# Performance work log

Measured on AMD Instinct MI355X. Metric: run time of the kernel, lower is better.

## Reference

```python
import jax, jax.numpy as jnp
from jax import lax
import numpy as np

B, H, W = 8, 160, 256
C, K = 700, 250
N_BINS = 750
N_HIST, N_JIT = 30, 60
N_FRAMES = N_HIST + N_JIT
MAGIC = 400.0 / (750.0 - 500.0 + 500.0)


def setup_inputs() -> dict:
    key = jax.random.key(0)
    ks = jax.random.split(key, 10)
    n_pix = H * W
    return {
        "batched_image": jax.random.normal(ks[0], (B, H, W), jnp.float32),
        "batched_spikes": jax.random.uniform(ks[1], (B, C, N_BINS), jnp.float32),
        "eye_movements": jax.random.randint(ks[2], (B, N_JIT, 2), 0, 15),
        "time_mask": jax.random.uniform(ks[3], (B, N_BINS - K), jnp.float32),
        "forward_sel": jax.random.randint(ks[4], (B, N_BINS, 2), 0, N_FRAMES),
        "forward_weights": jax.random.uniform(ks[5], (B, N_BINS, 2), jnp.float32),
        # scale filters so the generator signal stays O(1) under exp() nonlinearity
        "stacked_flat_spat_filters": jax.random.normal(ks[6], (C, n_pix), jnp.float32) / np.sqrt(n_pix).astype(np.float32),
        "stacked_timecourse_filters": jax.random.normal(ks[7], (C, K), jnp.float32) / np.sqrt(K).astype(np.float32),
        "precomputed_feedback_gensig": 0.1 * jax.random.normal(ks[8], (B, C, N_BINS - K + 1), jnp.float32),
        "precomputed_history_frames": jax.random.normal(ks[9], (B, N_HIST, C), jnp.float32),
    }


def _jitter(image, eye_movements):
    # image: (B,H,W); eye_movements: (B,F,2) int shifts. Gather with zero fill.
    dy, dx = eye_movements[..., 0], eye_movements[..., 1]
    rows = jnp.arange(H)[None, None, :] + dy[:, :, None]      # (B,F,H)
    cols = jnp.arange(W)[None, None, :] + dx[:, :, None]      # (B,F,W)
    vr = (rows >= 0) & (rows < H)
    vc = (cols >= 0) & (cols < W)
    rc = jnp.clip(rows, 0, H - 1)
    cc = jnp.clip(cols, 0, W - 1)
    bidx = jnp.arange(image.shape[0])[:, None, None, None]
    jit = image[bidx, rc[:, :, :, None], cc[:, :, None, :]]   # (B,F,H,W)
    mask = (vr[:, :, :, None] & vc[:, :, None, :]).astype(image.dtype)
    return jit * mask


def reference(batched_image, batched_spikes, eye_movements, time_mask,
              forward_sel, forward_weights, stacked_flat_spat_filters,
              stacked_timecourse_filters, precomputed_feedback_gensig,
              precomputed_history_frames):
    b = batched_image.shape[0]
    # eye-movement jitter (gather)
    jit = _jitter(batched_image, eye_movements)                       # (B,Fj,H,W)
    jit_flat = jit.reshape(b, -1, H * W)                              # (B,Fj,P)
    spat_j = jnp.einsum('cp,bfp->bfc', stacked_flat_spat_filters, jit_flat)
    spat = jnp.concatenate([precomputed_history_frames, spat_j], axis=1)  # (B,Ftot,C)
    # interval-overlap time upsample: each bin mixes <=2 frames
    t = forward_sel.shape[1]
    gath = jnp.take_along_axis(spat, forward_sel.reshape(b, t * 2, 1), axis=1)
    gath = gath.reshape(b, t, 2, -1)                                  # (B,T,2,C)
    upsampled = jnp.einsum('btjc,btj->bct', gath, forward_weights)    # (B,C,T)
    # grouped (depthwise) conv1d, valid, no flip (cross-correlation like torch)
    time_filt = lax.conv_general_dilated(
        upsampled, stacked_timecourse_filters[:, None, :],
        window_strides=(1,), padding='VALID',
        dimension_numbers=('NCH', 'OIH', 'NCH'), feature_group_count=C)  # (B,C,T-K+1)
    gen_sig = time_filt + precomputed_feedback_gensig
    g = gen_sig[:, :, :-1]
    s = batched_spikes[:, :, K:]
    loss = jnp.exp(g) - s * g                                          # Poisson NLL (unnormed)
    loss = loss * time_mask[:, None, :] * MAGIC
    return jnp.sum(loss, axis=(1, 2))
```

## Files before the change

kernel.cpp:

```cpp
#include <hip/hip_runtime.h>
#include <hip/hip_bf16.h>
#include <math.h>

#define BB    8
#define HH    160
#define WW    256
#define CC    700
#define KK    250
#define NBINS 750
#define NHIST 30
#define NJIT  60
#define NFRM  90
#define PP    (HH*WW)
#define TOUT  500
#define MAGIC (400.0f/750.0f)

#define MPAD   512
#define NPAD   768
#define KPTOT  640
#define KSPLIT 32
#define KPZ    20
#define BSCALE     64.0f
#define INV_BSCALE (1.0f/64.0f)
#define PA_BLKS (32*20)
#define PB_BLKS (48*20)

typedef __attribute__((ext_vector_type(8))) short short8;
typedef __attribute__((ext_vector_type(4))) float f32x4;

__device__ __forceinline__ unsigned char f2fp8(float x) {
    x = fminf(fmaxf(x, -440.f), 440.f);
    unsigned u = __builtin_bit_cast(unsigned, x);
    unsigned s = (u >> 24) & 0x80u;
    int e = (u >> 23) & 0xFF;
    if (e < 121) return (unsigned char)s;
    unsigned u2 = u + 0x7FFFFu + ((u >> 20) & 1u);
    int e2 = (u2 >> 23) & 0xFF;
    unsigned m = (u2 >> 20) & 7u;
    if (e2 > 135 || (e2 == 135 && m == 7u)) return (unsigned char)(s | 0x7E);
    return (unsigned char)(s | ((unsigned)(e2 - 120) << 3) | m);
}

__device__ __forceinline__ unsigned pk4_fp8(float a, float b, float c, float d) {
#if __has_builtin(__builtin_amdgcn_cvt_pk_fp8_f32)
    int v = __builtin_amdgcn_cvt_pk_fp8_f32(a, b, 0, false);
    v = __builtin_amdgcn_cvt_pk_fp8_f32(c, d, v, true);
    return (unsigned)v;
#else
    return (unsigned)f2fp8(a) | ((unsigned)f2fp8(b) << 8)
         | ((unsigned)f2fp8(c) << 16) | ((unsigned)f2fp8(d) << 24);
#endif
}

__device__ __forceinline__ void gload16(const void* g, void* l) {
    __builtin_amdgcn_global_load_lds(
        (const __attribute__((address_space(1))) unsigned int*)g,
        (__attribute__((address_space(3))) unsigned int*)l, 16, 0, 0);
}

__device__ __forceinline__ int SWZ(int X) { return X ^ (((X >> 8) & 7) << 4); }

__device__ __forceinline__ int FRX(int r, int pl) {
    return ((pl >> 6) << 10) | ((((pl >> 3) & 3) * 16 + r) << 4)
         | (((pl >> 5) & 1) << 3) | (pl & 7);
}

__global__ __launch_bounds__(256) void pack_ab(
    const float* __restrict__ img, const int* __restrict__ eye,
    const float* __restrict__ filt,
    unsigned char* __restrict__ Ap, unsigned char* __restrict__ Bp)
{
    __shared__ unsigned char lds[8192];
    const int t = threadIdx.x, w = t >> 6, l = t & 63;
    const int bid = blockIdx.x;

    if (bid < PA_BLKS) {
        const int mt = bid / 20, ch4 = bid % 20;
        int rbv[4], rdy[4], rdx[4]; bool rok[4];
        #pragma unroll
        for (int sub = 0; sub < 4; ++sub) {
            int r = sub*4 + w, m = mt*16 + r;
            rok[sub] = (m < 480);
            int b = 0, dy = 0, dx = 0;
            if (rok[sub]) {
                b = m / 60; int f = m % 60;
                dy = eye[(b*NJIT + f)*2 + 0];
                dx = eye[(b*NJIT + f)*2 + 1];
            }
            rbv[sub] = b; rdy[sub] = dy; rdx[sub] = dx;
        }
        for (int q = 0; q < 4; ++q) {
            const int ch = ch4*4 + q;
            const int kbase = ch * 512;
            #pragma unroll
            for (int sub = 0; sub < 4; ++sub) {
                const int r = sub*4 + w;
                const float* imgb = img + (size_t)rbv[sub]*PP;
                const int dx = rdx[sub];
                #pragma unroll
                for (int h = 0; h < 2; ++h) {
                    const int ir = (kbase >> 8) + h + rdy[sub];
                    const bool ok = rok[sub] && (ir < HH);
                    float4 v = make_float4(0.f,0.f,0.f,0.f);
                    if (ok) v = *(const float4*)(imgb + ir*WW + 4*l);
                    unsigned pk = pk4_fp8(v.x, v.y, v.z, v.w);
                    const int plb = h*256;
                    if (!ok || l >= 60)
                        *(unsigned*)(lds + SWZ(FRX(r, plb + 4*l))) = 0u;
                    if (ok) {
                        #pragma unroll
                        for (int j = 0; j < 4; ++j) {
                            int pc = 4*l + j - dx;
                            if (pc >= 0)
                                lds[SWZ(FRX(r, plb + pc))] =
                                    (unsigned char)(pk >> (8*j));
                        }
                    }
                }
            }
            __syncthreads();
            unsigned char* outp = Ap + ((size_t)mt*KPTOT + ch*8)*1024;
            #pragma unroll
            for (int i = 0; i < 2; ++i) {
                int X = i*4096 + t*16;
                short8 v = *(const short8*)(lds + SWZ(X));
                *(short8*)(outp + X) = v;
            }
            __syncthreads();
        }
    } else {
        const int bb = bid - PA_BLKS;
        const int nt = bb / 20, ch4 = bb % 20;
        for (int q = 0; q < 4; ++q) {
            const int ch = ch4*4 + q;
            const int kbase = ch * 512;
            #pragma unroll
            for (int sub = 0; sub < 4; ++sub) {
                int r = sub*4 + w, n = nt*16 + r;
                float4 va = make_float4(0.f,0.f,0.f,0.f), vb = va;
                if (n < CC) {
                    const float* rowp = filt + (size_t)n*PP + kbase;
                    va = *(const float4*)(rowp + l*4);
                    vb = *(const float4*)(rowp + l*4 + 256);
                }
                unsigned da = pk4_fp8(va.x*BSCALE, va.y*BSCALE, va.z*BSCALE, va.w*BSCALE);
                unsigned db = pk4_fp8(vb.x*BSCALE, vb.y*BSCALE, vb.z*BSCALE, vb.w*BSCALE);
                int Xa = FRX(r, 4*l);
                *(unsigned*)(lds + SWZ(Xa)) = da;
                *(unsigned*)(lds + SWZ(Xa + (4 << 10))) = db;
            }
            __syncthreads();
            unsigned char* outp = Bp + ((size_t)nt*KPTOT + ch*8)*1024;
            #pragma unroll
            for (int i = 0; i < 2; ++i) {
                int X = i*4096 + t*16;
                short8 v = *(const short8*)(lds + SWZ(X));
                *(short8*)(outp + X) = v;
            }
            __syncthreads();
        }
    }
}

__global__ __launch_bounds__(256) void gemm_f8(
    const unsigned char* __restrict__ Ap, const unsigned char* __restrict__ Bp,
    __hip_bfloat16* __restrict__ part)
{
    __shared__ unsigned char As[8192];
    __shared__ unsigned char Bs[8192];

    const int t = threadIdx.x, l = t & 63, w = t >> 6;
    const int bid = blockIdx.x;
    const int g   = bid >> 3;
    const int z   = (bid & 7) + 8*(g / 24);
    const int tt  = g % 24;
    const int mtile = tt / 6, ntile = tt % 6;
    const int wr = w >> 1, wc = w & 1;

    f32x4 acc[4][4] = {};

    for (int step = 0; step < KPZ; ++step) {
        const size_t kp = (size_t)z*KPZ + step;
        const int tb0 = w*2, tb1 = w*2 + 1;
        gload16(Ap + ((size_t)(mtile*8 + tb0)*KPTOT + kp)*1024 + l*16, As + tb0*1024);
        gload16(Ap + ((size_t)(mtile*8 + tb1)*KPTOT + kp)*1024 + l*16, As + tb1*1024);
        gload16(Bp + ((size_t)(ntile*8 + tb0)*KPTOT + kp)*1024 + l*16, Bs + tb0*1024);
        gload16(Bp + ((size_t)(ntile*8 + tb1)*KPTOT + kp)*1024 + l*16, Bs + tb1*1024);
        __syncthreads();

        ulonglong2 a[4], b[4];
        #pragma unroll
        for (int i = 0; i < 4; ++i)
            a[i] = *(const ulonglong2*)(As + (wr*4 + i)*1024 + l*16);
        #pragma unroll
        for (int j = 0; j < 4; ++j)
            b[j] = *(const ulonglong2*)(Bs + (wc*4 + j)*1024 + l*16);
        #pragma unroll
        for (int i = 0; i < 4; ++i)
            #pragma unroll
            for (int j = 0; j < 4; ++j) {
                acc[i][j] = __builtin_amdgcn_mfma_f32_16x16x32_fp8_fp8(
                    (long long)a[i].x, (long long)b[j].x, acc[i][j], 0, 0, 0);
                acc[i][j] = __builtin_amdgcn_mfma_f32_16x16x32_fp8_fp8(
                    (long long)a[i].y, (long long)b[j].y, acc[i][j], 0, 0, 0);
            }
        __syncthreads();
    }

    const int rbase = (l >> 4)*4, cl = l & 15;
    #pragma unroll
    for (int i = 0; i < 4; ++i)
        #pragma unroll
        for (int j = 0; j < 4; ++j) {
            int m = mtile*128 + wr*64 + i*16 + rbase;
            int n = ntile*128 + wc*64 + j*16 + cl;
            __hip_bfloat16* p = part + ((size_t)z*MPAD + m)*NPAD + n;
            #pragma unroll
            for (int r = 0; r < 4; ++r)
                p[(size_t)r*NPAD] = __float2bfloat16(acc[i][j][r]);
        }
}

__global__ __launch_bounds__(256) void build_spat(
    const float* __restrict__ hist, const __hip_bfloat16* __restrict__ part,
    float* __restrict__ spat)
{
    int idx = blockIdx.x*256 + threadIdx.x;
    if (idx >= BB*NFRM*CC) return;
    int c   = idx % CC;
    int rem = idx / CC;
    int fr  = rem % NFRM;
    int b   = rem / NFRM;
    float v;
    if (fr < NHIST) {
        v = hist[(b*NHIST + fr)*CC + c];
    } else {
        int m = b*NJIT + (fr - NHIST);
        v = 0.f;
        #pragma unroll
        for (int kp = 0; kp < KSPLIT; ++kp)
            v += __bfloat162float(part[((size_t)kp*MPAD + m)*NPAD + c]);
        v *= INV_BSCALE;
    }
    spat[idx] = v;
}

__global__ __launch_bounds__(64) void conv_loss(
    const float* __restrict__ spat, const int* __restrict__ sel,
    const float* __restrict__ wts,  const float* __restrict__ tc,
    const float* __restrict__ fb,   const float* __restrict__ spk,
    const float* __restrict__ tmask, float* __restrict__ lpart)
{
    __shared__ float tcs[256];
    __shared__ float ups[864];

    const int lane = threadIdx.x;
    const int c = blockIdx.x;
    const int b = blockIdx.y;

    for (int k = lane; k < 256; k += 64)
        tcs[k] = (k < KK) ? tc[c*KK + k] : 0.f;

    const float* spb = spat + (size_t)b*NFRM*CC + c;
    for (int tt = lane; tt < 768; tt += 64) {
        float v = 0.f;
        if (tt < NBINS) {
            int base = (b*NBINS + tt)*2;
            int s0 = sel[base], s1 = sel[base+1];
            float w0 = wts[base], w1 = wts[base+1];
            v = w0 * spb[s0*CC] + w1 * spb[s1*CC];
        }
        ups[tt + (tt >> 3)] = v;
    }
    __syncthreads();

    const int t0 = lane * 8;
    float u[16];
    #pragma unroll
    for (int j = 0; j < 16; ++j) { int q = t0 + j; u[j] = ups[q + (q >> 3)]; }

    float acc[8] = {};
    #pragma unroll 4
    for (int kc = 0; kc < 248; kc += 8) {
        #pragma unroll
        for (int kk = 0; kk < 8; ++kk) {
            float w2 = tcs[kc + kk];
            #pragma unroll
            for (int j = 0; j < 8; ++j) acc[j] += w2 * u[kk + j];
        }
        #pragma unroll
        for (int j = 0; j < 8; ++j) u[j] = u[j + 8];
        #pragma unroll
        for (int j = 0; j < 8; ++j) {
            int q = t0 + kc + 16 + j;
            u[j + 8] = ups[q + (q >> 3)];
        }
    }
    #pragma unroll
    for (int kk = 0; kk < 8; ++kk) {
        float w2 = tcs[248 + kk];
        #pragma unroll
        for (int j = 0; j < 8; ++j) acc[j] += w2 * u[kk + j];
    }

    const size_t bc = (size_t)b*CC + c;
    const float* fbp = fb  + bc*(TOUT+1);
    const float* sp  = spk + bc*NBINS + KK;
    const float* tm  = tmask + (size_t)b*TOUT;
    float lsum = 0.f;
    #pragma unroll
    for (int j = 0; j < 8; ++j) {
        int tt = t0 + j;
        if (tt < TOUT) {
            float g  = acc[j] + fbp[tt];
            float sv = sp[tt];
            lsum += (__expf(g) - sv*g) * tm[tt];
        }
    }
    #pragma unroll
    for (int off = 32; off > 0; off >>= 1)
        lsum += __shfl_down(lsum, off);
    if (lane == 0) lpart[bc] = lsum * MAGIC;
}

__global__ __launch_bounds__(256) void reduce_out(
    const float* __restrict__ lpart, float* __restrict__ out)
{
    __shared__ float red[256];
    int b = blockIdx.x, t = threadIdx.x;
    float s = 0.f;
    for (int i = t; i < CC; i += 256) s += lpart[(size_t)b*CC + i];
    red[t] = s; __syncthreads();
    for (int o = 128; o > 0; o >>= 1) {
        if (t < o) red[t] += red[t+o];
        __syncthreads();
    }
    if (t == 0) out[b] = red[0];
}

extern "C" void kernel_launch(void* const* d_in, const int* in_sizes, int n_in,
                              void* d_out, int out_size, void* d_ws, size_t ws_size,
                              hipStream_t stream) {
    const float* image = (const float*)d_in[0];
    const float* spk   = (const float*)d_in[1];
    const int*   eye   = (const int*)d_in[2];
    const float* tmask = (const float*)d_in[3];
    const int*   sel   = (const int*)d_in[4];
    const float* wts   = (const float*)d_in[5];
    const float* filt  = (const float*)d_in[6];
    const float* tc    = (const float*)d_in[7];
    const float* fb    = (const float*)d_in[8];
    const float* hist  = (const float*)d_in[9];
    float* out = (float*)d_out;

    unsigned char* Ap = (unsigned char*)d_ws;
    unsigned char* Bp = Ap + (size_t)32*KPTOT*1024;
    __hip_bfloat16* part = (__hip_bfloat16*)(Bp + (size_t)48*KPTOT*1024);
    float* spat  = (float*)(part + (size_t)KSPLIT*MPAD*NPAD);
    float* lpart = spat + (size_t)BB*NFRM*CC;

    pack_ab  <<<dim3(PA_BLKS + PB_BLKS), 256, 0, stream>>>(image, eye, filt, Ap, Bp);
    gemm_f8  <<<dim3(8*96), 256, 0, stream>>>(Ap, Bp, part);
    build_spat<<<dim3((BB*NFRM*CC + 255)/256), 256, 0, stream>>>(hist, part, spat);
    conv_loss<<<dim3(CC, BB), 64, 0, stream>>>(spat, sel, wts, tc, fb, spk, tmask, lpart);
    reduce_out<<<dim3(BB), 256, 0, stream>>>(lpart, out);
}
```

Baseline: 113.3 us.

## Direct-pack filter operand per thread and transpose spat for per-channel LDS gather

```diff
diff --git a/kernel.cpp b/kernel.cpp
--- a/kernel.cpp
+++ b/kernel.cpp
@@ -23,7 +23,7 @@
 #define BSCALE     64.0f
 #define INV_BSCALE (1.0f/64.0f)
 #define PA_BLKS (32*20)
-#define PB_BLKS (48*20)
+#define PBD_BLKS ((768*640)/256)
 
 typedef __attribute__((ext_vector_type(8))) short short8;
 typedef __attribute__((ext_vector_type(4))) float f32x4;
@@ -129,35 +129,28 @@
             __syncthreads();
         }
     } else {
-        const int bb = bid - PA_BLKS;
-        const int nt = bb / 20, ch4 = bb % 20;
-        for (int q = 0; q < 4; ++q) {
-            const int ch = ch4*4 + q;
-            const int kbase = ch * 512;
-            #pragma unroll
-            for (int sub = 0; sub < 4; ++sub) {
-                int r = sub*4 + w, n = nt*16 + r;
-                float4 va = make_float4(0.f,0.f,0.f,0.f), vb = va;
-                if (n < CC) {
-                    const float* rowp = filt + (size_t)n*PP + kbase;
-                    va = *(const float4*)(rowp + l*4);
-                    vb = *(const float4*)(rowp + l*4 + 256);
-                }
-                unsigned da = pk4_fp8(va.x*BSCALE, va.y*BSCALE, va.z*BSCALE, va.w*BSCALE);
-                unsigned db = pk4_fp8(vb.x*BSCALE, vb.y*BSCALE, vb.z*BSCALE, vb.w*BSCALE);
-                int Xa = FRX(r, 4*l);
-                *(unsigned*)(lds + SWZ(Xa)) = da;
-                *(unsigned*)(lds + SWZ(Xa + (4 << 10))) = db;
-            }
-            __syncthreads();
-            unsigned char* outp = Bp + ((size_t)nt*KPTOT + ch*8)*1024;
-            #pragma unroll
-            for (int i = 0; i < 2; ++i) {
-                int X = i*4096 + t*16;
-                short8 v = *(const short8*)(lds + SWZ(X));
-                *(short8*)(outp + X) = v;
-            }
-            __syncthreads();
+        const int tidg = (bid - PA_BLKS)*256 + t;
+        const int kp = tidg % KPTOT;
+        const int r  = tidg / KPTOT;
+        const int nt = r >> 4, rloc = r & 15;
+        const bool ok = (r < CC);
+        const float* rp = filt + (size_t)(ok ? r : 0)*PP + kp*64;
+        unsigned char* op = Bp + ((size_t)nt*KPTOT + kp)*1024 + rloc*16;
+        #pragma unroll
+        for (int hi = 0; hi < 2; ++hi) {
+            float4 fv[8];
+            #pragma unroll
+            for (int qd = 0; qd < 8; ++qd)
+                fv[qd] = ok ? *(const float4*)(rp + hi*32 + qd*4)
+                            : make_float4(0.f,0.f,0.f,0.f);
+            #pragma unroll
+            for (int quad = 0; quad < 4; ++quad) {
+                float4 a = fv[quad*2], b2 = fv[quad*2+1];
+                uint2 dv;
+                dv.x = pk4_fp8(a.x*BSCALE,  a.y*BSCALE,  a.z*BSCALE,  a.w*BSCALE);
+                dv.y = pk4_fp8(b2.x*BSCALE, b2.y*BSCALE, b2.z*BSCALE, b2.w*BSCALE);
+                *(uint2*)(op + quad*256 + hi*8) = dv;
+            }
         }
     }
 }
@@ -223,7 +216,7 @@
 
 __global__ __launch_bounds__(256) void build_spat(
     const float* __restrict__ hist, const __hip_bfloat16* __restrict__ part,
-    float* __restrict__ spat)
+    float* __restrict__ spatT)
 {
     int idx = blockIdx.x*256 + threadIdx.x;
     if (idx >= BB*NFRM*CC) return;
@@ -242,16 +235,17 @@
             v += __bfloat162float(part[((size_t)kp*MPAD + m)*NPAD + c]);
         v *= INV_BSCALE;
     }
-    spat[idx] = v;
+    spatT[((size_t)b*CC + c)*NFRM + fr] = v;
 }
 
 __global__ __launch_bounds__(64) void conv_loss(
-    const float* __restrict__ spat, const int* __restrict__ sel,
+    const float* __restrict__ spatT, const int* __restrict__ sel,
     const float* __restrict__ wts,  const float* __restrict__ tc,
     const float* __restrict__ fb,   const float* __restrict__ spk,
     const float* __restrict__ tmask, float* __restrict__ lpart)
 {
     __shared__ float tcs[256];
+    __shared__ float spc[96];
     __shared__ float ups[864];
 
     const int lane = threadIdx.x;
@@ -260,15 +254,19 @@
 
     for (int k = lane; k < 256; k += 64)
         tcs[k] = (k < KK) ? tc[c*KK + k] : 0.f;
-
-    const float* spb = spat + (size_t)b*NFRM*CC + c;
+    {
+        const float* spT = spatT + (size_t)(b*CC + c)*NFRM;
+        for (int i = lane; i < NFRM; i += 64) spc[i] = spT[i];
+    }
+    __syncthreads();
+
     for (int tt = lane; tt < 768; tt += 64) {
         float v = 0.f;
         if (tt < NBINS) {
-            int base = (b*NBINS + tt)*2;
-            int s0 = sel[base], s1 = sel[base+1];
-            float w0 = wts[base], w1 = wts[base+1];
-            v = w0 * spb[s0*CC] + w1 * spb[s1*CC];
+            int base = (b*NBINS + tt);
+            int2   s2 = *(const int2*)  (sel + base*2);
+            float2 w2 = *(const float2*)(wts + base*2);
+            v = w2.x * spc[s2.x] + w2.y * spc[s2.y];
         }
         ups[tt + (tt >> 3)] = v;
     }
@@ -356,12 +354,12 @@
     unsigned char* Ap = (unsigned char*)d_ws;
     unsigned char* Bp = Ap + (size_t)32*KPTOT*1024;
     __hip_bfloat16* part = (__hip_bfloat16*)(Bp + (size_t)48*KPTOT*1024);
-    float* spat  = (float*)(part + (size_t)KSPLIT*MPAD*NPAD);
-    float* lpart = spat + (size_t)BB*NFRM*CC;
-
-    pack_ab  <<<dim3(PA_BLKS + PB_BLKS), 256, 0, stream>>>(image, eye, filt, Ap, Bp);
+    float* spatT = (float*)(part + (size_t)KSPLIT*MPAD*NPAD);
+    float* lpart = spatT + (size_t)BB*NFRM*CC;
+
+    pack_ab  <<<dim3(PA_BLKS + PBD_BLKS), 256, 0, stream>>>(image, eye, filt, Ap, Bp);
     gemm_f8  <<<dim3(8*96), 256, 0, stream>>>(Ap, Bp, part);
-    build_spat<<<dim3((BB*NFRM*CC + 255)/256), 256, 0, stream>>>(hist, part, spat);
-    conv_loss<<<dim3(CC, BB), 64, 0, stream>>>(spat, sel, wts, tc, fb, spk, tmask, lpart);
+    build_spat<<<dim3((BB*NFRM*CC + 255)/256), 256, 0, stream>>>(hist, part, spatT);
+    conv_loss<<<dim3(CC, BB), 64, 0, stream>>>(spatT, sel, wts, tc, fb, spk, tmask, lpart);
     reduce_out<<<dim3(BB), 256, 0, stream>>>(lpart, out);
 }
```

After: 221.9 us. 1.96x slower.
